# Kernel tuning notes

Measured on AMD Instinct MI355X. Metric: run time of the kernel, lower is better.

The kernel has to match this reference:

```python
import jax, jax.numpy as jnp
import numpy as np

H = 256       # hidden_dim
E = H // 2    # operator embedding dim
T = 12        # num_tempers
O = 3         # num_ops per temper
HOPS = 4      # max_path_hops
B = 128       # batch
D = 2048      # input_dim
NCLS = 10     # task_head classes


def setup_inputs() -> dict:
    key = jax.random.key(0)
    ks = jax.random.split(key, 12)
    x = jax.random.normal(ks[0], (B, D), jnp.float32)
    N = B * (D // H)  # 1024 patch tokens
    # per-hop routed temper per patch; value == T means halt
    sampled_tempers = jax.random.randint(ks[1], (HOPS, N), 0, T + 1, jnp.int32)
    sampled_ops = jax.random.randint(ks[2], (HOPS, N), 0, O, jnp.int32)
    s1 = 1.0 / np.sqrt(H + E)
    W1 = jax.random.uniform(ks[3], (T, O, H + E, H), jnp.float32, -s1, s1)
    b1 = jax.random.uniform(ks[4], (T, O, H), jnp.float32, -s1, s1)
    s2 = 1.0 / np.sqrt(H)
    W2 = jax.random.uniform(ks[5], (T, O, H, H), jnp.float32, -s2, s2)
    b2 = jax.random.uniform(ks[6], (T, O, H), jnp.float32, -s2, s2)
    op_emb = jax.random.normal(ks[7], (T, O, E), jnp.float32)
    ln_g = jnp.ones((H,), jnp.float32)
    ln_b = jnp.zeros((H,), jnp.float32)
    Wt = jax.random.uniform(ks[8], (H, NCLS), jnp.float32, -s2, s2)
    bt = jax.random.uniform(ks[9], (NCLS,), jnp.float32, -s2, s2)
    return dict(x=x, W1=W1, b1=b1, W2=W2, b2=b2, op_emb=op_emb,
                ln_g=ln_g, ln_b=ln_b, Wt=Wt, bt=bt,
                sampled_tempers=sampled_tempers, sampled_ops=sampled_ops)


def reference(x, W1, b1, W2, b2, op_emb, ln_g, ln_b, Wt, bt,
              sampled_tempers, sampled_ops):
    Bsz, Din = x.shape
    pad = (-Din) % H
    if pad > 0:
        x = jnp.pad(x, ((0, 0), (0, pad)))
    state = x.reshape(-1, H)                       # [N, H] patch states
    active = jnp.ones((state.shape[0],), bool)     # not-yet-halted mask
    for hop in range(HOPS):
        t = sampled_tempers[hop]
        o = sampled_ops[hop]
        active = active & (t != T)                 # T == halt action
        tc = jnp.clip(t, 0, T - 1)                 # safe index for halted rows
        emb = op_emb[tc, o]                        # [N, E] op embedding gather
        xa = jnp.concatenate([state, emb], axis=-1)  # [N, H+E]
        # per-token expert weight gather + batched matvec (memory-bound dispatch)
        h = jax.nn.relu(jnp.einsum('ni,nio->no', xa, W1[tc, o]) + b1[tc, o])
        y = jax.nn.relu(jnp.einsum('ni,nio->no', h, W2[tc, o]) + b2[tc, o])
        state = jnp.where(active[:, None], y, state)
    pooled = state.reshape(Bsz, -1, H).mean(axis=1)   # [B, H]
    mu = pooled.mean(axis=-1, keepdims=True)
    var = pooled.var(axis=-1, keepdims=True)
    normed = (pooled - mu) * jax.lax.rsqrt(var + 1e-5) * ln_g + ln_b
    return normed @ Wt + bt                           # [B, 10]
```

## Files before the change

### kernel.cpp

```cpp
#include <hip/hip_runtime.h>

typedef __attribute__((ext_vector_type(8))) short short8;
typedef __attribute__((ext_vector_type(4))) float floatx4;

#define NEXP   36
#define NTOK   1024
#define HOPS   4

#define OFF_STATE   0u
#define OFF_W1B     1048576u
#define OFF_W2B     5767168u
#define OFF_C1      10485760u
#define OFF_COUNTS  10522624u
#define OFF_LISTS   10523264u
#define OFF_JOBS    11113088u
#define OFF_NJ      11115136u

__device__ __forceinline__ unsigned short f2bf(float f) {
    unsigned u = __float_as_uint(f);
    u += 0x7FFFu + ((u >> 16) & 1u);
    return (unsigned short)(u >> 16);
}

__global__ __launch_bounds__(256) void prep_kernel(
    const float* __restrict__ x, const float* __restrict__ W1,
    const float* __restrict__ b1, const float* __restrict__ W2,
    const float* __restrict__ op_emb,
    const int* __restrict__ tempers, const int* __restrict__ ops,
    float* __restrict__ state, unsigned short* __restrict__ W1b,
    unsigned short* __restrict__ W2b, float* __restrict__ c1,
    int* __restrict__ counts, int* __restrict__ lists,
    int* __restrict__ jobs, int* __restrict__ njobs)
{
    const int bid = blockIdx.x;
    const int t = threadIdx.x;

    if (bid < 2304) {
        const int mat = bid / 1152;
        const int id  = bid % 1152;
        const int e   = id / 32;
        const int sub = id % 32;
        const int kb  = sub / 4;
        const int jt  = sub % 4;
        const float* src = mat ? (W2 + e * 65536) : (W1 + e * 98304);
        unsigned short* dst = (mat ? W2b : W1b) + e * 65536;
        const int j  = jt * 64 + (t & 63);
        const int ks = (t >> 6) * 8;
        short8 v;
        #pragma unroll
        for (int i = 0; i < 8; i++)
            v[i] = (short)f2bf(src[(kb * 32 + ks + i) * 256 + j]);
        *(short8*)(dst + (kb * 256 + j) * 32 + ks) = v;
    } else if (bid < 2340) {
        const int e = bid - 2304;
        __shared__ float eb[128];
        if (t < 128) eb[t] = op_emb[e * 128 + t];
        __syncthreads();
        float acc = b1[e * 256 + t];
        const float* wp = W1 + e * 98304 + 256 * 256;
        #pragma unroll 4
        for (int k = 0; k < 128; k++)
            acc += eb[k] * wp[k * 256 + t];
        c1[e * 256 + t] = acc;
    } else if (bid < 2404) {
        const int cb = bid - 2340;
        const float4* xs = (const float4*)x;
        float4* ss = (float4*)state;
        #pragma unroll
        for (int p = 0; p < 4; p++) {
            int i4 = cb * 1024 + p * 256 + t;
            ss[i4] = xs[i4];
        }
    } else {
        __shared__ int lc[HOPS * NEXP];
        if (t < HOPS * NEXP) lc[t] = 0;
        __syncthreads();
        for (int q = 0; q < 4; q++) {
            int n = q * 256 + t;
            bool act = true;
            for (int hop = 0; hop < HOPS; hop++) {
                int tt = tempers[hop * NTOK + n];
                int oo = ops[hop * NTOK + n];
                act = act && (tt != 12);
                if (act) {
                    int e = tt * 3 + oo;
                    int pos = atomicAdd(&lc[hop * NEXP + e], 1);
                    lists[(hop * NEXP + e) * NTOK + pos] = n;
                }
            }
        }
        __syncthreads();
        if (t < HOPS * NEXP) counts[t] = lc[t];
        if (t < HOPS) {
            int hop = t, nj = 0;
            for (int e = 0; e < NEXP; e++) {
                int c = lc[hop * NEXP + e];
                for (int m0 = 0; m0 < c; m0 += 16)
                    jobs[hop * 128 + nj++] = (m0 << 8) | e;
            }
            njobs[hop] = nj;
        }
    }
}

__global__ __launch_bounds__(1024) void hop_kernel(
    float* __restrict__ state,
    const unsigned short* __restrict__ W1b,
    const unsigned short* __restrict__ W2b,
    const float* __restrict__ c1, const float* __restrict__ b2,
    const int* __restrict__ counts, const int* __restrict__ lists,
    const int* __restrict__ jobs, const int* __restrict__ njobs, int hop)
{
    if (blockIdx.x >= njobs[hop]) return;
    const int job = jobs[hop * 128 + blockIdx.x];
    const int e   = job & 0xFF;
    const int m0  = job >> 8;
    const int n_e = counts[hop * NEXP + e];
    const int mact = min(16, n_e - m0);

    __shared__ int toks[16];
    __shared__ unsigned short Ab[4096];
    __shared__ unsigned short Hb[4096];

    const int t = threadIdx.x;
    if (t < 16) toks[t] = (t < mact) ? lists[(hop * NEXP + e) * NTOK + m0 + t] : 0;
    __syncthreads();

    {
        int m = t >> 6;
        int k = (t & 63) * 4;
        float4 v = make_float4(0.f, 0.f, 0.f, 0.f);
        if (m < mact) v = *(const float4*)(state + toks[m] * 256 + k);
        int kb = k >> 5, g = (k >> 3) & 3, i = k & 7;
        unsigned short* d = Ab + kb * 512 + (g * 16 + m) * 8 + i;
        d[0] = f2bf(v.x); d[1] = f2bf(v.y); d[2] = f2bf(v.z); d[3] = f2bf(v.w);
    }
    __syncthreads();

    const int l = t & 63, w = t >> 6;
    const int col = l & 15, g = l >> 4;
    const int j = w * 16 + col;

    floatx4 acc;
    {
        float cv = c1[e * 256 + j];
        acc = (floatx4){cv, cv, cv, cv};
    }
    const unsigned short* Wp = W1b + e * 65536;
    #pragma unroll
    for (int kb = 0; kb < 8; kb++) {
        short8 a = *(const short8*)(Ab + kb * 512 + l * 8);
        short8 bfrg = *(const short8*)(Wp + (kb * 256 + j) * 32 + g * 8);
        acc = __builtin_amdgcn_mfma_f32_16x16x32_bf16(a, bfrg, acc, 0, 0, 0);
    }
    {
        int kh = j;
        int kb2 = kh >> 5, g2 = (kh >> 3) & 3, i2 = kh & 7;
        #pragma unroll
        for (int r = 0; r < 4; r++) {
            int m = g * 4 + r;
            float vv = acc[r];
            vv = vv > 0.f ? vv : 0.f;
            Hb[kb2 * 512 + (g2 * 16 + m) * 8 + i2] = f2bf(vv);
        }
    }
    __syncthreads();

    {
        float bv = b2[e * 256 + j];
        acc = (floatx4){bv, bv, bv, bv};
    }
    const unsigned short* Wp2 = W2b + e * 65536;
    #pragma unroll
    for (int kb = 0; kb < 8; kb++) {
        short8 a = *(const short8*)(Hb + kb * 512 + l * 8);
        short8 bfrg = *(const short8*)(Wp2 + (kb * 256 + j) * 32 + g * 8);
        acc = __builtin_amdgcn_mfma_f32_16x16x32_bf16(a, bfrg, acc, 0, 0, 0);
    }
    #pragma unroll
    for (int r = 0; r < 4; r++) {
        int m = g * 4 + r;
        if (m < mact) {
            float vv = acc[r];
            state[toks[m] * 256 + j] = vv > 0.f ? vv : 0.f;
        }
    }
}

__global__ __launch_bounds__(256) void final_kernel(
    const float* __restrict__ state, const float* __restrict__ ln_g,
    const float* __restrict__ ln_b, const float* __restrict__ Wt,
    const float* __restrict__ bt, float* __restrict__ out)
{
    const int b = blockIdx.x, t = threadIdx.x;
    float s = 0.f;
    #pragma unroll
    for (int p = 0; p < 8; p++) s += state[(b * 8 + p) * 256 + t];
    s *= 0.125f;

    float v1 = s, v2 = s * s;
    #pragma unroll
    for (int off = 32; off; off >>= 1) {
        v1 += __shfl_down(v1, off);
        v2 += __shfl_down(v2, off);
    }
    __shared__ float red[8];
    __shared__ float stats[2];
    const int w = t >> 6, l = t & 63;
    if (l == 0) { red[w] = v1; red[4 + w] = v2; }
    __syncthreads();
    if (t == 0) {
        float su = red[0] + red[1] + red[2] + red[3];
        float sq = red[4] + red[5] + red[6] + red[7];
        float mu = su * (1.0f / 256.0f);
        float var = sq * (1.0f / 256.0f) - mu * mu;
        stats[0] = mu;
        stats[1] = rsqrtf(var + 1e-5f);
    }
    __syncthreads();
    float normed = (s - stats[0]) * stats[1] * ln_g[t] + ln_b[t];

    __shared__ float pr[40];
    #pragma unroll
    for (int c = 0; c < 10; c++) {
        float pv = normed * Wt[t * 10 + c];
        #pragma unroll
        for (int off = 32; off; off >>= 1) pv += __shfl_down(pv, off);
        if (l == 0) pr[w * 10 + c] = pv;
    }
    __syncthreads();
    if (t < 10)
        out[b * 10 + t] = pr[t] + pr[10 + t] + pr[20 + t] + pr[30 + t] + bt[t];
}

extern "C" void kernel_launch(void* const* d_in, const int* in_sizes, int n_in,
                              void* d_out, int out_size, void* d_ws, size_t ws_size,
                              hipStream_t stream)
{
    const float* x      = (const float*)d_in[0];
    const float* W1     = (const float*)d_in[1];
    const float* b1     = (const float*)d_in[2];
    const float* W2     = (const float*)d_in[3];
    const float* b2     = (const float*)d_in[4];
    const float* op_emb = (const float*)d_in[5];
    const float* ln_g   = (const float*)d_in[6];
    const float* ln_b   = (const float*)d_in[7];
    const float* Wt     = (const float*)d_in[8];
    const float* bt     = (const float*)d_in[9];
    const int* tempers  = (const int*)d_in[10];
    const int* ops      = (const int*)d_in[11];

    char* ws = (char*)d_ws;
    float* state          = (float*)(ws + OFF_STATE);
    unsigned short* W1b   = (unsigned short*)(ws + OFF_W1B);
    unsigned short* W2b   = (unsigned short*)(ws + OFF_W2B);
    float* c1             = (float*)(ws + OFF_C1);
    int* counts           = (int*)(ws + OFF_COUNTS);
    int* lists            = (int*)(ws + OFF_LISTS);
    int* jobs             = (int*)(ws + OFF_JOBS);
    int* njobs            = (int*)(ws + OFF_NJ);
    float* out            = (float*)d_out;

    prep_kernel<<<2405, 256, 0, stream>>>(x, W1, b1, W2, op_emb, tempers, ops,
                                          state, W1b, W2b, c1, counts, lists,
                                          jobs, njobs);
    for (int hop = 0; hop < HOPS; hop++)
        hop_kernel<<<128, 1024, 0, stream>>>(state, W1b, W2b, c1, b2,
                                             counts, lists, jobs, njobs, hop);
    final_kernel<<<128, 256, 0, stream>>>(state, ln_g, ln_b, Wt, bt, out);
}
```

Measured before the change: 142.4 us.

## Assign one block per expert and keep expert weights in registers across tiles

Each hop kernel now launches one block per expert, not one block per 16-token job. The block loads that expert's W1 and W2 bf16 fragments into registers once and loops over all of the expert's token tiles. This removes the per-job weight reloads and the job-list construction in prep. In exchange only up to 36 blocks run per hop, which lowers parallelism, and experts with many tokens process their tiles serially.

After: 146.8 us. +3.1%, slower.

```diff
diff --git a/kernel.cpp b/kernel.cpp
--- a/kernel.cpp
+++ b/kernel.cpp
@@ -13,8 +13,6 @@
 #define OFF_C1      10485760u
 #define OFF_COUNTS  10522624u
 #define OFF_LISTS   10523264u
-#define OFF_JOBS    11113088u
-#define OFF_NJ      11115136u
 
 __device__ __forceinline__ unsigned short f2bf(float f) {
     unsigned u = __float_as_uint(f);
@@ -29,8 +27,7 @@
     const int* __restrict__ tempers, const int* __restrict__ ops,
     float* __restrict__ state, unsigned short* __restrict__ W1b,
     unsigned short* __restrict__ W2b, float* __restrict__ c1,
-    int* __restrict__ counts, int* __restrict__ lists,
-    int* __restrict__ jobs, int* __restrict__ njobs)
+    int* __restrict__ counts, int* __restrict__ lists)
 {
     const int bid = blockIdx.x;
     const int t = threadIdx.x;
@@ -91,15 +88,6 @@
         }
         __syncthreads();
         if (t < HOPS * NEXP) counts[t] = lc[t];
-        if (t < HOPS) {
-            int hop = t, nj = 0;
-            for (int e = 0; e < NEXP; e++) {
-                int c = lc[hop * NEXP + e];
-                for (int m0 = 0; m0 < c; m0 += 16)
-                    jobs[hop * 128 + nj++] = (m0 << 8) | e;
-            }
-            njobs[hop] = nj;
-        }
     }
 }
 
@@ -108,81 +96,82 @@
     const unsigned short* __restrict__ W1b,
     const unsigned short* __restrict__ W2b,
     const float* __restrict__ c1, const float* __restrict__ b2,
-    const int* __restrict__ counts, const int* __restrict__ lists,
-    const int* __restrict__ jobs, const int* __restrict__ njobs, int hop)
-{
-    if (blockIdx.x >= njobs[hop]) return;
-    const int job = jobs[hop * 128 + blockIdx.x];
-    const int e   = job & 0xFF;
-    const int m0  = job >> 8;
+    const int* __restrict__ counts, const int* __restrict__ lists, int hop)
+{
+    const int e   = blockIdx.x;
     const int n_e = counts[hop * NEXP + e];
-    const int mact = min(16, n_e - m0);
+    if (n_e == 0) return;
+
+    const int t = threadIdx.x;
+    const int l = t & 63, w = t >> 6;
+    const int col = l & 15, g = l >> 4;
+    const int j = w * 16 + col;
+
+    const unsigned short* Wp  = W1b + e * 65536;
+    const unsigned short* Wp2 = W2b + e * 65536;
+    short8 B1[8], B2[8];
+    #pragma unroll
+    for (int kb = 0; kb < 8; kb++) {
+        B1[kb] = *(const short8*)(Wp  + (kb * 256 + j) * 32 + g * 8);
+        B2[kb] = *(const short8*)(Wp2 + (kb * 256 + j) * 32 + g * 8);
+    }
+    const float cv = c1[e * 256 + j];
+    const float bv = b2[e * 256 + j];
 
     __shared__ int toks[16];
     __shared__ unsigned short Ab[4096];
     __shared__ unsigned short Hb[4096];
 
-    const int t = threadIdx.x;
-    if (t < 16) toks[t] = (t < mact) ? lists[(hop * NEXP + e) * NTOK + m0 + t] : 0;
-    __syncthreads();
-
-    {
-        int m = t >> 6;
-        int k = (t & 63) * 4;
-        float4 v = make_float4(0.f, 0.f, 0.f, 0.f);
-        if (m < mact) v = *(const float4*)(state + toks[m] * 256 + k);
-        int kb = k >> 5, g = (k >> 3) & 3, i = k & 7;
-        unsigned short* d = Ab + kb * 512 + (g * 16 + m) * 8 + i;
-        d[0] = f2bf(v.x); d[1] = f2bf(v.y); d[2] = f2bf(v.z); d[3] = f2bf(v.w);
-    }
-    __syncthreads();
-
-    const int l = t & 63, w = t >> 6;
-    const int col = l & 15, g = l >> 4;
-    const int j = w * 16 + col;
-
-    floatx4 acc;
-    {
-        float cv = c1[e * 256 + j];
-        acc = (floatx4){cv, cv, cv, cv};
-    }
-    const unsigned short* Wp = W1b + e * 65536;
-    #pragma unroll
-    for (int kb = 0; kb < 8; kb++) {
-        short8 a = *(const short8*)(Ab + kb * 512 + l * 8);
-        short8 bfrg = *(const short8*)(Wp + (kb * 256 + j) * 32 + g * 8);
-        acc = __builtin_amdgcn_mfma_f32_16x16x32_bf16(a, bfrg, acc, 0, 0, 0);
-    }
-    {
-        int kh = j;
-        int kb2 = kh >> 5, g2 = (kh >> 3) & 3, i2 = kh & 7;
+    const int* lp = lists + (hop * NEXP + e) * NTOK;
+
+    for (int m0 = 0; m0 < n_e; m0 += 16) {
+        const int mact = min(16, n_e - m0);
+        __syncthreads();
+        if (t < 16) toks[t] = (t < mact) ? lp[m0 + t] : 0;
+        __syncthreads();
+
+        {
+            int m = t >> 6;
+            int k = (t & 63) * 4;
+            float4 v = make_float4(0.f, 0.f, 0.f, 0.f);
+            if (m < mact) v = *(const float4*)(state + toks[m] * 256 + k);
+            int kb = k >> 5, gg = (k >> 3) & 3, i = k & 7;
+            unsigned short* d = Ab + kb * 512 + (gg * 16 + m) * 8 + i;
+            d[0] = f2bf(v.x); d[1] = f2bf(v.y); d[2] = f2bf(v.z); d[3] = f2bf(v.w);
+        }
+        __syncthreads();
+
+        floatx4 acc = (floatx4){cv, cv, cv, cv};
+        #pragma unroll
+        for (int kb = 0; kb < 8; kb++) {
+            short8 a = *(const short8*)(Ab + kb * 512 + l * 8);
+            acc = __builtin_amdgcn_mfma_f32_16x16x32_bf16(a, B1[kb], acc, 0, 0, 0);
+        }
+        {
+            int kb2 = j >> 5, g2 = (j >> 3) & 3, i2 = j & 7;
+            #pragma unroll
+            for (int r = 0; r < 4; r++) {
+                int m = g * 4 + r;
+                float vv = acc[r];
+                vv = vv > 0.f ? vv : 0.f;
+                Hb[kb2 * 512 + (g2 * 16 + m) * 8 + i2] = f2bf(vv);
+            }
+        }
+        __syncthreads();
+
+        floatx4 acc2 = (floatx4){bv, bv, bv, bv};
+        #pragma unroll
+        for (int kb = 0; kb < 8; kb++) {
+            short8 a = *(const short8*)(Hb + kb * 512 + l * 8);
+            acc2 = __builtin_amdgcn_mfma_f32_16x16x32_bf16(a, B2[kb], acc2, 0, 0, 0);
+        }
         #pragma unroll
         for (int r = 0; r < 4; r++) {
             int m = g * 4 + r;
-            float vv = acc[r];
-            vv = vv > 0.f ? vv : 0.f;
-            Hb[kb2 * 512 + (g2 * 16 + m) * 8 + i2] = f2bf(vv);
-        }
-    }
-    __syncthreads();
-
-    {
-        float bv = b2[e * 256 + j];
-        acc = (floatx4){bv, bv, bv, bv};
-    }
-    const unsigned short* Wp2 = W2b + e * 65536;
-    #pragma unroll
-    for (int kb = 0; kb < 8; kb++) {
-        short8 a = *(const short8*)(Hb + kb * 512 + l * 8);
-        short8 bfrg = *(const short8*)(Wp2 + (kb * 256 + j) * 32 + g * 8);
-        acc = __builtin_amdgcn_mfma_f32_16x16x32_bf16(a, bfrg, acc, 0, 0, 0);
-    }
-    #pragma unroll
-    for (int r = 0; r < 4; r++) {
-        int m = g * 4 + r;
-        if (m < mact) {
-            float vv = acc[r];
-            state[toks[m] * 256 + j] = vv > 0.f ? vv : 0.f;
+            if (m < mact) {
+                float vv = acc2[r];
+                state[toks[m] * 256 + j] = vv > 0.f ? vv : 0.f;
+            }
         }
     }
 }
@@ -257,15 +246,12 @@
     float* c1             = (float*)(ws + OFF_C1);
     int* counts           = (int*)(ws + OFF_COUNTS);
     int* lists            = (int*)(ws + OFF_LISTS);
-    int* jobs             = (int*)(ws + OFF_JOBS);
-    int* njobs            = (int*)(ws + OFF_NJ);
     float* out            = (float*)d_out;
 
     prep_kernel<<<2405, 256, 0, stream>>>(x, W1, b1, W2, op_emb, tempers, ops,
-                                          state, W1b, W2b, c1, counts, lists,
-                                          jobs, njobs);
+                                          state, W1b, W2b, c1, counts, lists);
     for (int hop = 0; hop < HOPS; hop++)
-        hop_kernel<<<128, 1024, 0, stream>>>(state, W1b, W2b, c1, b2,
-                                             counts, lists, jobs, njobs, hop);
+        hop_kernel<<<NEXP, 1024, 0, stream>>>(state, W1b, W2b, c1, b2,
+                                              counts, lists, hop);
     final_kernel<<<128, 256, 0, stream>>>(state, ln_g, ln_b, Wt, bt, out);
 }
```
